# Kernel tuning notes

Hardware: AMD Instinct MI355X
Metric: run time of the kernel (lower is better)

The kernel has to match this reference:

```python
import jax, jax.numpy as jnp
import numpy as np

SIGMA = 10.0   # collision energy prefactor (init kwarg sigma)
LCOL = 0.5     # collision length scale (init kwarg lcol)
N_CHAINS = 2
CONF_LEN = 16388  # 4 header entries + 2 * 8192 step angles


def _chain_energy(conf):
    # conf: (CONF_LEN,) ; entries 0..3 only feed a zeroed init position
    c = conf[4:] + 0.5                     # (2N,) in [0,1]
    r1, r2 = c[0::2], c[1::2]              # (N,), (N,)
    ph = r1 * (2.0 * jnp.pi)
    th = jnp.arccos(1.0 - 2.0 * r2)
    sth = jnp.sin(th)
    steps = jnp.stack([sth * jnp.cos(ph), sth * jnp.sin(ph), jnp.cos(th)], axis=1)  # (N,3) unit vectors
    steps = jnp.concatenate([jnp.zeros((1, 3), conf.dtype), steps], axis=0)        # prepend origin
    pos = jnp.cumsum(steps, axis=0)        # (M,3) polymer positions, M = N+1
    # squared pairwise distances via Gram trick: ||a-b||^2 = |a|^2 + |b|^2 - 2 a.b
    sq = jnp.sum(pos * pos, axis=1)        # (M,)
    d2 = sq[:, None] + sq[None, :] - 2.0 * (pos @ pos.T)  # (M,M)
    d2 = jnp.maximum(d2, 0.0)              # clamp fp negatives
    # torch: sigma * sum(exp(-(cdist/lcol)^2)) == sigma * sum(exp(-d2/lcol^2))
    return SIGMA * jnp.sum(jnp.exp(-d2 / (LCOL * LCOL)))


def setup_inputs() -> dict:
    key = jax.random.key(0)
    confdata = jax.random.uniform(key, (N_CHAINS, CONF_LEN), dtype=jnp.float32,
                                  minval=-0.5, maxval=0.5)
    return {"confdata": confdata}


def reference(confdata):
    # sum of per-chain energies (torch loops over chains and accumulates)
    return jnp.sum(jax.vmap(_chain_energy)(confdata))
```

## Files before the change

kernel.cpp:

```cpp
#include <hip/hip_runtime.h>
#include <math.h>

#define N_CHAINS 2
#define CONF_LEN 16388
#define NSTEPS   8192
#define NPOS     8193
#define TILE     256
#define NTILES   33
#define NPAD     (NTILES * TILE)
#define NPAIRT   (NTILES * (NTILES + 1) / 2)
#define SIGMA    10.0f

__device__ float4 g_pos[N_CHAINS * NPAD];

__global__ void init_out_kernel(float* out) {
    out[0] = 0.0f;
}

__global__ __launch_bounds__(256) void pos_kernel(const float* __restrict__ conf,
                                                  float4* __restrict__ pos) {
    const int chain = blockIdx.x;
    const float* c = conf + chain * CONF_LEN;
    const int t = threadIdx.x;
    const int PER = NSTEPS / 256;
    const float TWO_PI = 6.2831853071795864769f;

    float sx = 0.f, sy = 0.f, sz = 0.f;
    for (int m = 0; m < PER; ++m) {
        int k = t * PER + m;
        float r1 = c[4 + 2 * k] + 0.5f;
        float r2 = c[5 + 2 * k] + 0.5f;
        float ph = r1 * TWO_PI;
        float ct = 1.0f - 2.0f * r2;
        float st = sqrtf(fmaxf(0.f, 1.0f - ct * ct));
        float sp, cp;
        __sincosf(ph, &sp, &cp);
        sx += st * cp; sy += st * sp; sz += ct;
    }

    __shared__ float lsx[256], lsy[256], lsz[256];
    lsx[t] = sx; lsy[t] = sy; lsz[t] = sz;
    __syncthreads();

    float ox = 0.f, oy = 0.f, oz = 0.f;
    for (int k = 0; k < t; ++k) { ox += lsx[k]; oy += lsy[k]; oz += lsz[k]; }

    float cx = ox, cy = oy, cz = oz;
    float4* cpos = pos + chain * NPAD;
    if (t == 0) cpos[0] = make_float4(0.f, 0.f, 0.f, 0.f);
    for (int m = 0; m < PER; ++m) {
        int k = t * PER + m;
        float r1 = c[4 + 2 * k] + 0.5f;
        float r2 = c[5 + 2 * k] + 0.5f;
        float ph = r1 * TWO_PI;
        float ct = 1.0f - 2.0f * r2;
        float st = sqrtf(fmaxf(0.f, 1.0f - ct * ct));
        float sp, cp;
        __sincosf(ph, &sp, &cp);
        cx += st * cp; cy += st * sp; cz += ct;
        float B = -4.0f * (cx * cx + cy * cy + cz * cz);
        cpos[k + 1] = make_float4(cx, cy, cz, B);
    }

    for (int idx = NPOS + t; idx < NPAD; idx += 256) {
        cpos[idx] = make_float4(0.f, 0.f, 0.f, -1.0e30f);
    }
}

__global__ __launch_bounds__(256) void pair_kernel(const float4* __restrict__ pos,
                                                   float* __restrict__ out) {
    int b = blockIdx.x;
    const int chain = b / NPAIRT;
    int p = b % NPAIRT;
    int ti = 0;
    while (true) {
        int rowlen = NTILES - ti;
        if (p < rowlen) break;
        p -= rowlen;
        ++ti;
    }
    const int tj = ti + p;

    const int t = threadIdx.x;
    const float4* cpos = pos + chain * NPAD;

    __shared__ float4 sj[TILE];
    sj[t] = cpos[tj * TILE + t];
    __syncthreads();

    const float4 pi4 = cpos[ti * TILE + t];
    const float xi = pi4.x, yi = pi4.y, zi = pi4.z, Ai = pi4.w;

    float acc = 0.f;
#pragma unroll 8
    for (int j = 0; j < TILE; ++j) {
        float4 q = sj[j];
        float dot = fmaf(xi, q.x, fmaf(yi, q.y, zi * q.z));
        float E = fmaf(8.0f, dot, Ai) + q.w;
        acc += __expf(E);
    }

    const float w = (ti == tj) ? 1.0f : 2.0f;
    acc *= w * SIGMA;

    for (int off = 32; off > 0; off >>= 1) acc += __shfl_down(acc, off, 64);
    __shared__ float wsum[4];
    if ((t & 63) == 0) wsum[t >> 6] = acc;
    __syncthreads();
    if (t == 0) {
        float s = wsum[0] + wsum[1] + wsum[2] + wsum[3];
        atomicAdd(out, s);
    }
}

extern "C" void kernel_launch(void* const* d_in, const int* in_sizes, int n_in,
                              void* d_out, int out_size, void* d_ws, size_t ws_size,
                              hipStream_t stream) {
    const float* conf = (const float*)d_in[0];
    float* out = (float*)d_out;

    float4* pos;
    hipGetSymbolAddress((void**)&pos, HIP_SYMBOL(g_pos));

    init_out_kernel<<<1, 1, 0, stream>>>(out);
    pos_kernel<<<N_CHAINS, 256, 0, stream>>>(conf, pos);
    pair_kernel<<<N_CHAINS * NPAIRT, 256, 0, stream>>>(pos, out);
}
```

Baseline: 90.89 us.

## Cull distant tile pairs via AABBs, rescale for exp2, parallelise prefix scan

The position kernel now runs 1024 threads per chain with a wave-shuffle prefix scan and vectorised float4 loads. It pre-scales coordinates so the pair energy reduces to a single exp2. It also computes per-tile bounding boxes, which the pair kernel uses to skip tile pairs whose minimum distance makes every exponential term negligible. The separate init kernel and hipGetSymbolAddress call are removed. Skipping far tiles drops contributions that fall below a cutoff, which is an approximation, but their size is well below float precision of the sum.

```diff
diff --git a/kernel.cpp b/kernel.cpp
--- a/kernel.cpp
+++ b/kernel.cpp
@@ -10,79 +10,146 @@
 #define NPAD     (NTILES * TILE)
 #define NPAIRT   (NTILES * (NTILES + 1) / 2)
 #define SIGMA    10.0f
+#define ALPHA    3.3972887f
+#define D2CUT    460.0f
+#define PTHREADS 1024
+#define NPAIRS   4096
+#define ROWS     (NPAIRS / PTHREADS)
 
 __device__ float4 g_pos[N_CHAINS * NPAD];
+__device__ float4 g_aabb_min[N_CHAINS * NTILES];
+__device__ float4 g_aabb_max[N_CHAINS * NTILES];
 
-__global__ void init_out_kernel(float* out) {
-    out[0] = 0.0f;
+__device__ __forceinline__ float exp2_fast(float x) {
+#if __has_builtin(__builtin_amdgcn_exp2f)
+    return __builtin_amdgcn_exp2f(x);
+#else
+    return exp2f(x);
+#endif
 }
 
-__global__ __launch_bounds__(256) void pos_kernel(const float* __restrict__ conf,
-                                                  float4* __restrict__ pos) {
+__global__ __launch_bounds__(1024) void pos_kernel(const float* __restrict__ conf,
+                                                   float* __restrict__ out) {
     const int chain = blockIdx.x;
-    const float* c = conf + chain * CONF_LEN;
     const int t = threadIdx.x;
-    const int PER = NSTEPS / 256;
+    const int lane = t & 63;
+    const int w = t >> 6;
     const float TWO_PI = 6.2831853071795864769f;
 
-    float sx = 0.f, sy = 0.f, sz = 0.f;
-    for (int m = 0; m < PER; ++m) {
-        int k = t * PER + m;
-        float r1 = c[4 + 2 * k] + 0.5f;
-        float r2 = c[5 + 2 * k] + 0.5f;
-        float ph = r1 * TWO_PI;
-        float ct = 1.0f - 2.0f * r2;
-        float st = sqrtf(fmaxf(0.f, 1.0f - ct * ct));
-        float sp, cp;
-        __sincosf(ph, &sp, &cp);
-        sx += st * cp; sy += st * sp; sz += ct;
+    const float4* cin = (const float4*)(conf + chain * CONF_LEN + 4);
+    float4* cpos = g_pos + chain * NPAD;
+
+    __shared__ float lds[48];
+
+    if (chain == 0 && t == 0) out[0] = 0.0f;
+    if (t == 0) cpos[0] = make_float4(0.f, 0.f, 0.f, 0.f);
+
+    float Rx = 0.f, Ry = 0.f, Rz = 0.f;
+
+    for (int m = 0; m < ROWS; ++m) {
+        const int p = t + PTHREADS * m;
+        float4 q = cin[p];
+
+        float sp0, cp0, sp1, cp1;
+        __sincosf((q.x + 0.5f) * TWO_PI, &sp0, &cp0);
+        float ct0 = 1.0f - 2.0f * (q.y + 0.5f);
+        float st0 = sqrtf(fmaxf(0.f, 1.0f - ct0 * ct0));
+        __sincosf((q.z + 0.5f) * TWO_PI, &sp1, &cp1);
+        float ct1 = 1.0f - 2.0f * (q.w + 0.5f);
+        float st1 = sqrtf(fmaxf(0.f, 1.0f - ct1 * ct1));
+        float ux0 = st0 * cp0, uy0 = st0 * sp0, uz0 = ct0;
+        float ux1 = st1 * cp1, uy1 = st1 * sp1, uz1 = ct1;
+        float sx = ux0 + ux1, sy = uy0 + uy1, sz = uz0 + uz1;
+
+        float ix = sx, iy = sy, iz = sz;
+        for (int off = 1; off < 64; off <<= 1) {
+            float nx = __shfl_up(ix, off, 64);
+            float ny = __shfl_up(iy, off, 64);
+            float nz = __shfl_up(iz, off, 64);
+            if (lane >= off) { ix += nx; iy += ny; iz += nz; }
+        }
+        float ex = __shfl_up(ix, 1, 64);
+        float ey = __shfl_up(iy, 1, 64);
+        float ez = __shfl_up(iz, 1, 64);
+        if (lane == 0) { ex = 0.f; ey = 0.f; ez = 0.f; }
+        __syncthreads();
+        if (lane == 63) { lds[w] = ix; lds[16 + w] = iy; lds[32 + w] = iz; }
+        __syncthreads();
+        float wox = 0.f, woy = 0.f, woz = 0.f;
+        float tox = 0.f, toy = 0.f, toz = 0.f;
+        for (int w2 = 0; w2 < 16; ++w2) {
+            float ax = lds[w2], ay = lds[16 + w2], az = lds[32 + w2];
+            tox += ax; toy += ay; toz += az;
+            if (w2 < w) { wox += ax; woy += ay; woz += az; }
+        }
+
+        float bx = Rx + wox + ex, by = Ry + woy + ey, bz = Rz + woz + ez;
+        float x1 = bx + ux0, y1 = by + uy0, z1 = bz + uz0;
+        float x2 = bx + sx,  y2 = by + sy,  z2 = bz + sz;
+        float X1 = x1 * ALPHA, Y1 = y1 * ALPHA, Z1 = z1 * ALPHA;
+        float X2 = x2 * ALPHA, Y2 = y2 * ALPHA, Z2 = z2 * ALPHA;
+        float B1 = -0.5f * (X1 * X1 + Y1 * Y1 + Z1 * Z1);
+        float B2 = -0.5f * (X2 * X2 + Y2 * Y2 + Z2 * Z2);
+        cpos[2 * p + 1] = make_float4(X1, Y1, Z1, B1);
+        cpos[2 * p + 2] = make_float4(X2, Y2, Z2, B2);
+
+        Rx += tox; Ry += toy; Rz += toz;
     }
 
-    __shared__ float lsx[256], lsy[256], lsz[256];
-    lsx[t] = sx; lsy[t] = sy; lsz[t] = sz;
+    for (int idx = NPOS + t; idx < NPAD; idx += PTHREADS) {
+        cpos[idx] = make_float4(0.f, 0.f, 0.f, -1.0e30f);
+    }
     __syncthreads();
 
-    float ox = 0.f, oy = 0.f, oz = 0.f;
-    for (int k = 0; k < t; ++k) { ox += lsx[k]; oy += lsy[k]; oz += lsz[k]; }
-
-    float cx = ox, cy = oy, cz = oz;
-    float4* cpos = pos + chain * NPAD;
-    if (t == 0) cpos[0] = make_float4(0.f, 0.f, 0.f, 0.f);
-    for (int m = 0; m < PER; ++m) {
-        int k = t * PER + m;
-        float r1 = c[4 + 2 * k] + 0.5f;
-        float r2 = c[5 + 2 * k] + 0.5f;
-        float ph = r1 * TWO_PI;
-        float ct = 1.0f - 2.0f * r2;
-        float st = sqrtf(fmaxf(0.f, 1.0f - ct * ct));
-        float sp, cp;
-        __sincosf(ph, &sp, &cp);
-        cx += st * cp; cy += st * sp; cz += ct;
-        float B = -4.0f * (cx * cx + cy * cy + cz * cz);
-        cpos[k + 1] = make_float4(cx, cy, cz, B);
-    }
-
-    for (int idx = NPOS + t; idx < NPAD; idx += 256) {
-        cpos[idx] = make_float4(0.f, 0.f, 0.f, -1.0e30f);
+    for (int rep = 0; rep < 3; ++rep) {
+        if (rep == 2 && w != 0) break;
+        const int tau = (rep == 0) ? w : (rep == 1 ? w + 16 : 32);
+        float mnx = 1e30f, mny = 1e30f, mnz = 1e30f;
+        float mxx = -1e30f, mxy = -1e30f, mxz = -1e30f;
+        for (int j = 0; j < 4; ++j) {
+            float4 pt = cpos[tau * TILE + lane + 64 * j];
+            mnx = fminf(mnx, pt.x); mny = fminf(mny, pt.y); mnz = fminf(mnz, pt.z);
+            mxx = fmaxf(mxx, pt.x); mxy = fmaxf(mxy, pt.y); mxz = fmaxf(mxz, pt.z);
+        }
+        for (int off = 32; off > 0; off >>= 1) {
+            mnx = fminf(mnx, __shfl_down(mnx, off, 64));
+            mny = fminf(mny, __shfl_down(mny, off, 64));
+            mnz = fminf(mnz, __shfl_down(mnz, off, 64));
+            mxx = fmaxf(mxx, __shfl_down(mxx, off, 64));
+            mxy = fmaxf(mxy, __shfl_down(mxy, off, 64));
+            mxz = fmaxf(mxz, __shfl_down(mxz, off, 64));
+        }
+        if (lane == 0) {
+            g_aabb_min[chain * NTILES + tau] = make_float4(mnx, mny, mnz, 0.f);
+            g_aabb_max[chain * NTILES + tau] = make_float4(mxx, mxy, mxz, 0.f);
+        }
     }
 }
 
-__global__ __launch_bounds__(256) void pair_kernel(const float4* __restrict__ pos,
-                                                   float* __restrict__ out) {
+__global__ __launch_bounds__(256) void pair_kernel(float* __restrict__ out) {
     int b = blockIdx.x;
     const int chain = b / NPAIRT;
     int p = b % NPAIRT;
     int ti = 0;
     while (true) {
-        int rowlen = NTILES - ti;
-        if (p < rowlen) break;
-        p -= rowlen;
+        int rl = NTILES - ti;
+        if (p < rl) break;
+        p -= rl;
         ++ti;
     }
     const int tj = ti + p;
 
+    float4 mni = g_aabb_min[chain * NTILES + ti];
+    float4 mxi = g_aabb_max[chain * NTILES + ti];
+    float4 mnj = g_aabb_min[chain * NTILES + tj];
+    float4 mxj = g_aabb_max[chain * NTILES + tj];
+    float dx = fmaxf(0.f, fmaxf(mni.x - mxj.x, mnj.x - mxi.x));
+    float dy = fmaxf(0.f, fmaxf(mni.y - mxj.y, mnj.y - mxi.y));
+    float dz = fmaxf(0.f, fmaxf(mni.z - mxj.z, mnj.z - mxi.z));
+    if (fmaf(dx, dx, fmaf(dy, dy, dz * dz)) > D2CUT) return;
+
     const int t = threadIdx.x;
-    const float4* cpos = pos + chain * NPAD;
+    const float4* cpos = g_pos + chain * NPAD;
 
     __shared__ float4 sj[TILE];
     sj[t] = cpos[tj * TILE + t];
@@ -95,22 +162,17 @@
 #pragma unroll 8
     for (int j = 0; j < TILE; ++j) {
         float4 q = sj[j];
-        float dot = fmaf(xi, q.x, fmaf(yi, q.y, zi * q.z));
-        float E = fmaf(8.0f, dot, Ai) + q.w;
-        acc += __expf(E);
+        float E = fmaf(xi, q.x, fmaf(yi, q.y, fmaf(zi, q.z, Ai + q.w)));
+        acc += exp2_fast(E);
     }
 
-    const float w = (ti == tj) ? 1.0f : 2.0f;
-    acc *= w * SIGMA;
+    acc *= (ti == tj) ? SIGMA : 2.0f * SIGMA;
 
     for (int off = 32; off > 0; off >>= 1) acc += __shfl_down(acc, off, 64);
     __shared__ float wsum[4];
     if ((t & 63) == 0) wsum[t >> 6] = acc;
     __syncthreads();
-    if (t == 0) {
-        float s = wsum[0] + wsum[1] + wsum[2] + wsum[3];
-        atomicAdd(out, s);
-    }
+    if (t == 0) atomicAdd(out, wsum[0] + wsum[1] + wsum[2] + wsum[3]);
 }
 
 extern "C" void kernel_launch(void* const* d_in, const int* in_sizes, int n_in,
@@ -119,10 +181,6 @@
     const float* conf = (const float*)d_in[0];
     float* out = (float*)d_out;
 
-    float4* pos;
-    hipGetSymbolAddress((void**)&pos, HIP_SYMBOL(g_pos));
-
-    init_out_kernel<<<1, 1, 0, stream>>>(out);
-    pos_kernel<<<N_CHAINS, 256, 0, stream>>>(conf, pos);
-    pair_kernel<<<N_CHAINS * NPAIRT, 256, 0, stream>>>(pos, out);
+    pos_kernel<<<N_CHAINS, PTHREADS, 0, stream>>>(conf, out);
+    pair_kernel<<<N_CHAINS * NPAIRT, TILE, 0, stream>>>(out);
 }
```

New measurement: 82.49 us. -9.2%, faster.
